# Kernel optimization log

Measured on AMD Instinct MI355X. Metric: run time of the kernel, lower is better.

Reference implementation:

```python
import jax, jax.numpy as jnp
import numpy as np


def setup_inputs() -> dict:
    key = jax.random.key(0)
    ks = jax.random.split(key, 7)
    S, B, I, H, L = 512, 64, 512, 1024, 4
    sI = 1.0 / np.sqrt(I)
    sH = 1.0 / np.sqrt(H)
    return {
        "x": jax.random.normal(ks[0], (S, B, I), jnp.float32),
        "Wx0": jax.random.normal(ks[1], (I, 4 * H), jnp.float32) * sI,
        "Wh0": jax.random.normal(ks[2], (H, 4 * H), jnp.float32) * sH,
        "b0": jax.random.normal(ks[3], (4 * H,), jnp.float32) * 0.01,
        "Wx_rest": jax.random.normal(ks[4], (L - 1, H, 4 * H), jnp.float32) * sH,
        "Wh_rest": jax.random.normal(ks[5], (L - 1, H, 4 * H), jnp.float32) * sH,
        "b_rest": jax.random.normal(ks[6], (L - 1, 4 * H), jnp.float32) * 0.01,
    }


def _lstm_cell(xt, h, c, Wx, Wh, b):
    # gates packed as [i, f, g, o] along last dim; b = b_i + b_h (always summed in original)
    z = xt @ Wx + h @ Wh + b  # [B, 4H]
    i, f, g, o = jnp.split(z, 4, axis=-1)
    c_new = jax.nn.sigmoid(f) * c + jax.nn.sigmoid(i) * jnp.tanh(g)
    h_new = jax.nn.sigmoid(o) * jnp.tanh(c_new)
    return h_new, c_new


def reference(x, Wx0, Wh0, b0, Wx_rest, Wh_rest, b_rest):
    L = 1 + Wx_rest.shape[0]
    H = Wh0.shape[0]
    B = x.shape[1]

    def step(carry, xt):
        hs, cs = carry  # each [L, B, H]
        h_list, c_list = [], []
        inp = xt
        for l in range(L):
            Wx = Wx0 if l == 0 else Wx_rest[l - 1]
            Wh = Wh0 if l == 0 else Wh_rest[l - 1]
            b = b0 if l == 0 else b_rest[l - 1]
            h, c = _lstm_cell(inp, hs[l], cs[l], Wx, Wh, b)
            h_list.append(h)
            c_list.append(c)
            inp = h
        return (jnp.stack(h_list), jnp.stack(c_list)), inp

    h0 = jnp.zeros((L, B, H), x.dtype)
    c0 = jnp.zeros((L, B, H), x.dtype)
    (hL, cL), hidden_seq = jax.lax.scan(step, (h0, c0), x)
    # hidden_seq: [S, B, H] (matches torch cat+transpose result)
    # original concatenates per-layer [B,1,H] states along dim 0 -> [L*B, 1, H]
    h_layers = hL.reshape(L * B, 1, H)
    c_layers = cL.reshape(L * B, 1, H)
    return hidden_seq, (h_layers, c_layers)
```

## Files before the change

### kernel.cpp

```cpp
#include <hip/hip_runtime.h>
#include <hip/hip_bf16.h>
#include <math.h>


typedef _Float16 f16x8 __attribute__((ext_vector_type(8)));
typedef _Float16 f16x4 __attribute__((ext_vector_type(4)));
typedef float    f32x4 __attribute__((ext_vector_type(4)));

#define S_LEN 512
#define BATCH 64
#define HID   1024
#define GATES 4096
#define NCNT  8
#define CNT_STRIDE 32
#define CNT_PER_LAYER (2 * NCNT * CNT_STRIDE)


__global__ void conv_f32_f16(const float4* __restrict__ in,
                             f16x4* __restrict__ out, int n4) {
  int i = blockIdx.x * blockDim.x + threadIdx.x;
  if (i < n4) {
    float4 v = in[i];
    f16x4 o;
    o[0] = (_Float16)v.x; o[1] = (_Float16)v.y;
    o[2] = (_Float16)v.z; o[3] = (_Float16)v.w;
    out[i] = o;
  }
}

__global__ void conv_f16_f32(const f16x4* __restrict__ in,
                             float4* __restrict__ out, int n4) {
  int i = blockIdx.x * blockDim.x + threadIdx.x;
  if (i < n4) {
    f16x4 v = in[i];
    float4 o;
    o.x = (float)v[0]; o.y = (float)v[1];
    o.z = (float)v[2]; o.w = (float)v[3];
    out[i] = o;
  }
}

__global__ void transpose_w(const float* __restrict__ src, int srcK,
                            _Float16* __restrict__ dst, int dstStride, int dstOff) {
  __shared__ float tile[64][65];
  const int kc0 = blockIdx.y * 64;
  const int c0  = blockIdx.x * 64;
  const int tid = threadIdx.x;
  const int r4  = tid >> 6;
  const int cc  = tid & 63;
#pragma unroll
  for (int i = 0; i < 16; ++i) {
    int r = i * 4 + r4;
    tile[r][cc] = src[(size_t)(kc0 + r) * 4096 + c0 + cc];
  }
  __syncthreads();
#pragma unroll
  for (int i = 0; i < 16; ++i) {
    int c = i * 4 + r4;
    dst[(size_t)(c0 + c) * dstStride + dstOff + kc0 + cc] = (_Float16)tile[cc][c];
  }
}


__device__ __forceinline__ void bar_arrive(int* cnt, int bg, int cg) {
  __syncthreads();
  if (threadIdx.x == 0)
    __hip_atomic_fetch_add(&cnt[(bg * NCNT + (cg >> 4)) * CNT_STRIDE], 1,
                           __ATOMIC_RELAXED, __HIP_MEMORY_SCOPE_AGENT);
}

__device__ __forceinline__ void bar_wait(int* cnt, int bg, int phase) {
  if (threadIdx.x < NCNT) {
    const int target = phase * 16;
    while (__hip_atomic_load(&cnt[(bg * NCNT + threadIdx.x) * CNT_STRIDE],
                             __ATOMIC_RELAXED,
                             __HIP_MEMORY_SCOPE_AGENT) < target)
      __builtin_amdgcn_s_sleep(2);
  }
  __syncthreads();
}


template <int KX>
__launch_bounds__(256, 1)
__global__ void lstm_layer(const _Float16* __restrict__ inseq,
                           _Float16* outseq,
                           const _Float16* __restrict__ WT,
                           const float* __restrict__ bias,
                           float* __restrict__ hfin,
                           float* __restrict__ cfin,
                           int* __restrict__ flags) {
  constexpr int KTOT = KX + 1024;
  constexpr int XI = KX / 128;
  constexpr int HI = 8;

  const int tid  = threadIdx.x;
  const int lane = tid & 63;
  const int w    = tid >> 6;
  const int n    = lane & 15;
  const int q    = lane >> 4;
  const int cg   = blockIdx.x >> 1;
  const int bg   = blockIdx.x & 1;

  __shared__ float zred[4][32][33];

  f16x8 bx[XI][2], bh[HI][2];
#pragma unroll
  for (int ct = 0; ct < 2; ++ct) {
    const int p  = ct * 16 + n;
    const int sc = (p >> 3) * 1024 + cg * 8 + (p & 7);
    const _Float16* base = WT + (size_t)sc * KTOT;
#pragma unroll
    for (int i = 0; i < XI; ++i)
      bx[i][ct] = *(const f16x8*)(base + w * (KX / 4) + i * 32 + q * 8);
#pragma unroll
    for (int i = 0; i < HI; ++i)
      bh[i][ct] = *(const f16x8*)(base + KX + w * 256 + i * 32 + q * 8);
  }

  const int erow  = tid >> 3;
  const int ejl   = tid & 7;
  const int grow  = bg * 32 + erow;
  const int ghcol = cg * 8 + ejl;
  const float bi  = bias[ghcol];
  const float bf  = bias[1024 + ghcol];
  const float bgg = bias[2048 + ghcol];
  const float bo  = bias[3072 + ghcol];
  float creg = 0.0f;

  const int arow0 = bg * 32 + n;
  const int arow1 = bg * 32 + 16 + n;

  for (int t = 0; t < S_LEN; ++t) {
    f32x4 acc00 = {}, acc01 = {}, acc10 = {}, acc11 = {};

    {
      const _Float16* xt = inseq + (size_t)t * BATCH * KX;
      const _Float16* a0p = xt + (size_t)arow0 * KX + w * (KX / 4) + q * 8;
      const _Float16* a1p = xt + (size_t)arow1 * KX + w * (KX / 4) + q * 8;
#pragma unroll
      for (int i = 0; i < XI; ++i) {
        f16x8 a0 = *(const f16x8*)(a0p + i * 32);
        f16x8 a1 = *(const f16x8*)(a1p + i * 32);
        acc00 = __builtin_amdgcn_mfma_f32_16x16x32_f16(a0, bx[i][0], acc00, 0, 0, 0);
        acc01 = __builtin_amdgcn_mfma_f32_16x16x32_f16(a0, bx[i][1], acc01, 0, 0, 0);
        acc10 = __builtin_amdgcn_mfma_f32_16x16x32_f16(a1, bx[i][0], acc10, 0, 0, 0);
        acc11 = __builtin_amdgcn_mfma_f32_16x16x32_f16(a1, bx[i][1], acc11, 0, 0, 0);
      }
    }

    if (t > 0) {
      bar_wait(flags, bg, t);
      const _Float16* hp = outseq + (size_t)(t - 1) * BATCH * HID;
      const _Float16* a0p = hp + (size_t)arow0 * HID + w * 256 + q * 8;
      const _Float16* a1p = hp + (size_t)arow1 * HID + w * 256 + q * 8;
      f16x8 ha0[HI], ha1[HI];
#pragma unroll
      for (int i = 0; i < HI; ++i) {
        ha0[i] = *(const f16x8*)(a0p + i * 32);
        ha1[i] = *(const f16x8*)(a1p + i * 32);
      }
#pragma unroll
      for (int i = 0; i < HI; ++i) {
        acc00 = __builtin_amdgcn_mfma_f32_16x16x32_f16(ha0[i], bh[i][0], acc00, 0, 0, 0);
        acc01 = __builtin_amdgcn_mfma_f32_16x16x32_f16(ha0[i], bh[i][1], acc01, 0, 0, 0);
        acc10 = __builtin_amdgcn_mfma_f32_16x16x32_f16(ha1[i], bh[i][0], acc10, 0, 0, 0);
        acc11 = __builtin_amdgcn_mfma_f32_16x16x32_f16(ha1[i], bh[i][1], acc11, 0, 0, 0);
      }
    }

#pragma unroll
    for (int r = 0; r < 4; ++r) {
      zred[w][q * 4 + r][n]           = acc00[r];
      zred[w][q * 4 + r][16 + n]      = acc01[r];
      zred[w][16 + q * 4 + r][n]      = acc10[r];
      zred[w][16 + q * 4 + r][16 + n] = acc11[r];
    }
    __syncthreads();

    float zi = bi, zf = bf, zg = bgg, zo = bo;
#pragma unroll
    for (int ww = 0; ww < 4; ++ww) {
      zi += zred[ww][erow][ejl];
      zf += zred[ww][erow][8 + ejl];
      zg += zred[ww][erow][16 + ejl];
      zo += zred[ww][erow][24 + ejl];
    }
    float ig = 1.0f / (1.0f + __expf(-zi));
    float fg = 1.0f / (1.0f + __expf(-zf));
    float gg = tanhf(zg);
    float og = 1.0f / (1.0f + __expf(-zo));
    float cn = fg * creg + ig * gg;
    float h  = og * tanhf(cn);
    creg = cn;

    const size_t oidx = (size_t)grow * HID + ghcol;

    {
      _Float16 hh = (_Float16)h;
      unsigned short hb = __builtin_bit_cast(unsigned short, hh);
      unsigned short pb = (unsigned short)__shfl_xor((int)hb, 1, 64);
      if ((ejl & 1) == 0) {
        unsigned int packed = (unsigned int)hb | ((unsigned int)pb << 16);
        unsigned int* dst =
            (unsigned int*)(outseq + (size_t)t * BATCH * HID + oidx);
        __hip_atomic_store(dst, packed, __ATOMIC_RELAXED,
                           __HIP_MEMORY_SCOPE_AGENT);
      }
    }
    if (t == S_LEN - 1) { hfin[oidx] = h; cfin[oidx] = cn; }

    if (t + 1 < S_LEN) bar_arrive(flags, bg, cg);
    else __syncthreads();
  }
}


extern "C" void kernel_launch(void* const* d_in, const int* in_sizes, int n_in,
                              void* d_out, int out_size, void* d_ws, size_t ws_size,
                              hipStream_t stream) {
  const float* x_f32   = (const float*)d_in[0];
  const float* Wx0     = (const float*)d_in[1];
  const float* Wh0     = (const float*)d_in[2];
  const float* b0      = (const float*)d_in[3];
  const float* Wx_rest = (const float*)d_in[4];
  const float* Wh_rest = (const float*)d_in[5];
  const float* b_rest  = (const float*)d_in[6];

  float* out = (float*)d_out;
  float* hid_seq = out;
  float* h_fin   = out + (size_t)S_LEN * BATCH * HID;
  float* c_fin   = h_fin + (size_t)4 * BATCH * HID;

  size_t off = 0;
  auto alloc = [&](size_t bytes) {
    void* p = (char*)d_ws + off;
    off += (bytes + 255) & ~(size_t)255;
    return p;
  };
  _Float16* WT[4];
  WT[0] = (_Float16*)alloc((size_t)GATES * 1536 * 2);
  WT[1] = (_Float16*)alloc((size_t)GATES * 2048 * 2);
  WT[2] = (_Float16*)alloc((size_t)GATES * 2048 * 2);
  WT[3] = (_Float16*)alloc((size_t)GATES * 2048 * 2);
  _Float16* x16  = (_Float16*)alloc((size_t)S_LEN * BATCH * 512 * 2);
  _Float16* seq[4];
  for (int l = 0; l < 4; ++l)
    seq[l] = (_Float16*)alloc((size_t)S_LEN * BATCH * HID * 2);
  int* flags     = (int*)alloc(4 * CNT_PER_LAYER * sizeof(int));

  hipMemsetAsync(flags, 0, 4 * CNT_PER_LAYER * sizeof(int), stream);

  {
    int n4 = S_LEN * BATCH * 512 / 4;
    conv_f32_f16<<<dim3((n4 + 255) / 256), dim3(256), 0, stream>>>(
        (const float4*)x_f32, (f16x4*)x16, n4);
  }

  transpose_w<<<dim3(64, 512 / 64), dim3(256), 0, stream>>>(Wx0, 512, WT[0], 1536, 0);
  transpose_w<<<dim3(64, 1024 / 64), dim3(256), 0, stream>>>(Wh0, 1024, WT[0], 1536, 512);
  for (int l = 1; l < 4; ++l) {
    const float* wx = Wx_rest + (size_t)(l - 1) * 1024 * 4096;
    const float* wh = Wh_rest + (size_t)(l - 1) * 1024 * 4096;
    transpose_w<<<dim3(64, 1024 / 64), dim3(256), 0, stream>>>(wx, 1024, WT[l], 2048, 0);
    transpose_w<<<dim3(64, 1024 / 64), dim3(256), 0, stream>>>(wh, 1024, WT[l], 2048, 1024);
  }

  struct LayerCfg {
    const _Float16* in; _Float16* outp; const _Float16* wt; const float* b;
    float* hf; float* cf; int* flg; int kx;
  } cfg[4] = {
    { x16,    seq[0], WT[0], b0,              h_fin + 0 * 65536, c_fin + 0 * 65536, flags + 0 * CNT_PER_LAYER, 512 },
    { seq[0], seq[1], WT[1], b_rest + 0*4096, h_fin + 1 * 65536, c_fin + 1 * 65536, flags + 1 * CNT_PER_LAYER, 1024 },
    { seq[1], seq[2], WT[2], b_rest + 1*4096, h_fin + 2 * 65536, c_fin + 2 * 65536, flags + 2 * CNT_PER_LAYER, 1024 },
    { seq[2], seq[3], WT[3], b_rest + 2*4096, h_fin + 3 * 65536, c_fin + 3 * 65536, flags + 3 * CNT_PER_LAYER, 1024 },
  };

  for (int l = 0; l < 4; ++l) {
    const _Float16* pin = cfg[l].in;
    _Float16* pout = cfg[l].outp;
    const _Float16* pwt = cfg[l].wt;
    const float* pb = cfg[l].b;
    float* phf = cfg[l].hf;
    float* pcf = cfg[l].cf;
    int* pfl = cfg[l].flg;
    void* args[7] = { &pin, &pout, &pwt, &pb, &phf, &pcf, &pfl };
    if (cfg[l].kx == 512) {
      hipLaunchCooperativeKernel(reinterpret_cast<void*>(&lstm_layer<512>),
                                 dim3(256), dim3(256), args, 0, stream);
    } else {
      hipLaunchCooperativeKernel(reinterpret_cast<void*>(&lstm_layer<1024>),
                                 dim3(256), dim3(256), args, 0, stream);
    }
  }

  {
    int n4 = S_LEN * BATCH * HID / 4;
    conv_f16_f32<<<dim3((n4 + 255) / 256), dim3(256), 0, stream>>>(
        (const f16x4*)seq[3], (float4*)hid_seq, n4);
  }
}
```

Baseline: 14.27 ms.

## Replace block-level grid barrier with per-wave arrive/wait and double-buffered reduction smem

```diff
diff --git a/kernel.cpp b/kernel.cpp
--- a/kernel.cpp
+++ b/kernel.cpp
@@ -62,22 +62,22 @@
 }
 
 
-__device__ __forceinline__ void bar_arrive(int* cnt, int bg, int cg) {
-  __syncthreads();
-  if (threadIdx.x == 0)
+__device__ __forceinline__ void wave_arrive(int* cnt, int bg, int cg, int lane) {
+  asm volatile("s_waitcnt vmcnt(0)" ::: "memory");
+  if (lane == 0)
     __hip_atomic_fetch_add(&cnt[(bg * NCNT + (cg >> 4)) * CNT_STRIDE], 1,
                            __ATOMIC_RELAXED, __HIP_MEMORY_SCOPE_AGENT);
 }
 
-__device__ __forceinline__ void bar_wait(int* cnt, int bg, int phase) {
-  if (threadIdx.x < NCNT) {
-    const int target = phase * 16;
-    while (__hip_atomic_load(&cnt[(bg * NCNT + threadIdx.x) * CNT_STRIDE],
-                             __ATOMIC_RELAXED,
+__device__ __forceinline__ void wave_wait(int* cnt, int bg, int w, int lane,
+                                          int phase) {
+  const int target = phase * 64;
+  if (lane < 2) {
+    const int idx = (bg * NCNT + 2 * w + lane) * CNT_STRIDE;
+    while (__hip_atomic_load(&cnt[idx], __ATOMIC_RELAXED,
                              __HIP_MEMORY_SCOPE_AGENT) < target)
-      __builtin_amdgcn_s_sleep(2);
-  }
-  __syncthreads();
+      __builtin_amdgcn_s_sleep(1);
+  }
 }
 
 
@@ -102,7 +102,7 @@
   const int cg   = blockIdx.x >> 1;
   const int bg   = blockIdx.x & 1;
 
-  __shared__ float zred[4][32][33];
+  __shared__ float zred[2][4][32][36];
 
   f16x8 bx[XI][2], bh[HI][2];
 #pragma unroll
@@ -132,6 +132,7 @@
   const int arow1 = bg * 32 + 16 + n;
 
   for (int t = 0; t < S_LEN; ++t) {
+    const int par = t & 1;
     f32x4 acc00 = {}, acc01 = {}, acc10 = {}, acc11 = {};
 
     {
@@ -150,7 +151,7 @@
     }
 
     if (t > 0) {
-      bar_wait(flags, bg, t);
+      wave_wait(flags, bg, w, lane, t);
       const _Float16* hp = outseq + (size_t)(t - 1) * BATCH * HID;
       const _Float16* a0p = hp + (size_t)arow0 * HID + w * 256 + q * 8;
       const _Float16* a1p = hp + (size_t)arow1 * HID + w * 256 + q * 8;
@@ -171,20 +172,20 @@
 
 #pragma unroll
     for (int r = 0; r < 4; ++r) {
-      zred[w][q * 4 + r][n]           = acc00[r];
-      zred[w][q * 4 + r][16 + n]      = acc01[r];
-      zred[w][16 + q * 4 + r][n]      = acc10[r];
-      zred[w][16 + q * 4 + r][16 + n] = acc11[r];
+      zred[par][w][q * 4 + r][n]           = acc00[r];
+      zred[par][w][q * 4 + r][16 + n]      = acc01[r];
+      zred[par][w][16 + q * 4 + r][n]      = acc10[r];
+      zred[par][w][16 + q * 4 + r][16 + n] = acc11[r];
     }
     __syncthreads();
 
     float zi = bi, zf = bf, zg = bgg, zo = bo;
 #pragma unroll
     for (int ww = 0; ww < 4; ++ww) {
-      zi += zred[ww][erow][ejl];
-      zf += zred[ww][erow][8 + ejl];
-      zg += zred[ww][erow][16 + ejl];
-      zo += zred[ww][erow][24 + ejl];
+      zi += zred[par][ww][erow][ejl];
+      zf += zred[par][ww][erow][8 + ejl];
+      zg += zred[par][ww][erow][16 + ejl];
+      zo += zred[par][ww][erow][24 + ejl];
     }
     float ig = 1.0f / (1.0f + __expf(-zi));
     float fg = 1.0f / (1.0f + __expf(-zf));
@@ -210,8 +211,7 @@
     }
     if (t == S_LEN - 1) { hfin[oidx] = h; cfin[oidx] = cn; }
 
-    if (t + 1 < S_LEN) bar_arrive(flags, bg, cg);
-    else __syncthreads();
+    if (t + 1 < S_LEN) wave_arrive(flags, bg, cg, lane);
   }
 }
 
```

Result: no change. 14.37 ms (+0.7%).
